# Performance work log

Measured on AMD Instinct MI355X. Metric: run time of the kernel, lower is better.

The kernel has to match this reference:

```python
import jax, jax.numpy as jnp
import numpy as np

B, S, D, N_OPS = 16, 8192, 128, 4


def setup_inputs() -> dict:
    key = jax.random.key(0)
    k1, k2, k3 = jax.random.split(key, 3)
    x = jax.random.normal(k1, (B, S, D), dtype=jnp.float32)
    # candidate op parameters: 4 Linear(D, D) layers, stacked
    W = jax.random.normal(k2, (N_OPS, D, D), dtype=jnp.float32) * (1.0 / np.sqrt(D))
    b = jax.random.normal(k3, (N_OPS, D), dtype=jnp.float32) * 0.01
    # one-hot path selector buffer: weights[0] = 1.0 (as in MixModule.__init__)
    weights = jnp.zeros((N_OPS,), dtype=jnp.float32).at[0].set(1.0)
    return {"x": x, "W": W, "b": b, "weights": weights}


def reference(x, W, b, weights):
    # Faithful to the torch loop: compute EVERY candidate op(x), then the
    # weighted (one-hot) sum. outs: [B, S, n_ops, D]
    outs = jnp.einsum("bsd,ofd->bsof", x, W) + b[None, None, :, :]
    y = jnp.einsum("bsof,o->bsf", outs, weights)
    return y
```

## Files before the change

### kernel.cpp

```cpp
#include <hip/hip_runtime.h>
#include <hip/hip_bf16.h>

#define D 128
#define NOPS 4
#define BS_STRIDE 136
#define ROWS_PER_BLOCK 128

typedef __attribute__((ext_vector_type(8))) short short8;
typedef __attribute__((ext_vector_type(4))) float float4_t;

__global__ void combine_kernel(const float* __restrict__ W,
                               const float* __restrict__ b,
                               const float* __restrict__ wts,
                               __hip_bfloat16* __restrict__ Wc,
                               float* __restrict__ bc) {
    int idx = blockIdx.x * blockDim.x + threadIdx.x;
    float w0 = wts[0], w1 = wts[1], w2 = wts[2], w3 = wts[3];
    if (idx < D * D) {
        float v = w0 * W[idx] + w1 * W[D * D + idx]
                + w2 * W[2 * D * D + idx] + w3 * W[3 * D * D + idx];
        Wc[idx] = __float2bfloat16(v);
    }
    if (idx < D) {
        bc[idx] = w0 * b[idx] + w1 * b[D + idx] + w2 * b[2 * D + idx] + w3 * b[3 * D + idx];
    }
}

__device__ inline short8 cvt8_bf16(float4_t a, float4_t b) {
    union { short8 s; __hip_bfloat16 h[8]; } u;
    u.h[0] = __float2bfloat16(a[0]);
    u.h[1] = __float2bfloat16(a[1]);
    u.h[2] = __float2bfloat16(a[2]);
    u.h[3] = __float2bfloat16(a[3]);
    u.h[4] = __float2bfloat16(b[0]);
    u.h[5] = __float2bfloat16(b[1]);
    u.h[6] = __float2bfloat16(b[2]);
    u.h[7] = __float2bfloat16(b[3]);
    return u.s;
}

__global__ __launch_bounds__(512, 8) void gemm_kernel(const float* __restrict__ x,
                                                      const __hip_bfloat16* __restrict__ Wc,
                                                      const float* __restrict__ bc,
                                                      float* __restrict__ y,
                                                      int M) {
    __shared__ __align__(16) __hip_bfloat16 Bs[D * BS_STRIDE];

    const int tid   = threadIdx.x;
    const int lane  = tid & 63;
    const int wave  = tid >> 6;
    const int wslab = wave >> 1;
    const int whalf = wave & 1;

    #pragma unroll
    for (int i = 0; i < 4; i++) {
        int c  = i * 512 + tid;
        int n  = c >> 4;
        int ko = (c & 15) << 3;
        short8 v = *(const short8*)((const short*)Wc + n * D + ko);
        *(short8*)((short*)Bs + n * BS_STRIDE + ko) = v;
    }
    __syncthreads();

    const int row  = lane & 15;
    const int quad = lane >> 4;

    const int mbase = blockIdx.x * ROWS_PER_BLOCK + wslab * 16 + row;
    if (mbase >= M) return;

    const short* bp0 = (const short*)Bs + (whalf * 64 + row) * BS_STRIDE + quad * 8;

    #pragma unroll
    for (int s = 0; s < 2; s++) {
        const int m = mbase + s * 64;

        const float* xp = x + (size_t)m * D + quad * 8;
        short8 xf[4];
        #pragma unroll
        for (int ks = 0; ks < 4; ks++) {
            float4_t a0 = *(const float4_t*)(xp + ks * 32);
            float4_t a1 = *(const float4_t*)(xp + ks * 32 + 4);
            xf[ks] = cvt8_bf16(a0, a1);
        }

        float4_t acc[4];
        #pragma unroll
        for (int i = 0; i < 4; i++) acc[i] = (float4_t)(0.f);

        #pragma unroll
        for (int ks = 0; ks < 4; ks++) {
            #pragma unroll
            for (int f = 0; f < 4; f++) {
                short8 wfrag = *(const short8*)(bp0 + f * 16 * BS_STRIDE + ks * 32);
                acc[f] = __builtin_amdgcn_mfma_f32_16x16x32_bf16(wfrag, xf[ks], acc[f], 0, 0, 0);
            }
        }

        float* yp = y + (size_t)m * D + whalf * 64 + quad * 4;
        #pragma unroll
        for (int f = 0; f < 4; f++) {
            float4_t bias = *(const float4_t*)(bc + whalf * 64 + f * 16 + quad * 4);
            float4_t out;
            out[0] = acc[f][0] + bias[0];
            out[1] = acc[f][1] + bias[1];
            out[2] = acc[f][2] + bias[2];
            out[3] = acc[f][3] + bias[3];
            __builtin_nontemporal_store(out, (float4_t*)(yp + f * 16));
        }
    }
}

extern "C" void kernel_launch(void* const* d_in, const int* in_sizes, int n_in,
                              void* d_out, int out_size, void* d_ws, size_t ws_size,
                              hipStream_t stream) {
    const float* x   = (const float*)d_in[0];
    const float* W   = (const float*)d_in[1];
    const float* b   = (const float*)d_in[2];
    const float* wts = (const float*)d_in[3];
    float* y = (float*)d_out;

    __hip_bfloat16* Wc = (__hip_bfloat16*)d_ws;
    float* bc = (float*)((char*)d_ws + D * D * sizeof(__hip_bfloat16));

    combine_kernel<<<(D * D + 255) / 256, 256, 0, stream>>>(W, b, wts, Wc, bc);

    const int M = in_sizes[0] / D;
    gemm_kernel<<<M / ROWS_PER_BLOCK, 512, 0, stream>>>(x, Wc, bc, y, M);
}
```

Before: 128.0 us.

## Double-buffer x loads across four row slabs with XOR-swizzled weight LDS

Each block now covers 256 rows in four 64-row slabs per wave pair, prefetching the next slab's fp32 x into registers while the current slab runs its MFMAs. Padded LDS rows are replaced by an XOR swizzle to avoid bank conflicts without extra LDS. Output stores become ordinary stores instead of nontemporal, and launch bounds drop to 4 blocks per CU. The extra register buffers lower occupancy and halve the number of blocks, trading latency hiding by parallelism for explicit prefetch.

```diff
diff --git a/kernel.cpp b/kernel.cpp
--- a/kernel.cpp
+++ b/kernel.cpp
@@ -2,9 +2,8 @@
 #include <hip/hip_bf16.h>
 
 #define D 128
-#define NOPS 4
-#define BS_STRIDE 136
-#define ROWS_PER_BLOCK 128
+#define NSLAB 4
+#define ROWS_PER_BLOCK 256
 
 typedef __attribute__((ext_vector_type(8))) short short8;
 typedef __attribute__((ext_vector_type(4))) float float4_t;
@@ -39,48 +38,68 @@
     return u.s;
 }
 
-__global__ __launch_bounds__(512, 8) void gemm_kernel(const float* __restrict__ x,
+__global__ __launch_bounds__(512, 4) void gemm_kernel(const float* __restrict__ x,
                                                       const __hip_bfloat16* __restrict__ Wc,
                                                       const float* __restrict__ bc,
                                                       float* __restrict__ y,
                                                       int M) {
-    __shared__ __align__(16) __hip_bfloat16 Bs[D * BS_STRIDE];
+    __shared__ __align__(16) __hip_bfloat16 Bs[D * D];
 
     const int tid   = threadIdx.x;
     const int lane  = tid & 63;
     const int wave  = tid >> 6;
     const int wslab = wave >> 1;
     const int whalf = wave & 1;
+    const int r     = lane & 15;
+    const int quad  = lane >> 4;
 
     #pragma unroll
     for (int i = 0; i < 4; i++) {
-        int c  = i * 512 + tid;
-        int n  = c >> 4;
-        int ko = (c & 15) << 3;
-        short8 v = *(const short8*)((const short*)Wc + n * D + ko);
-        *(short8*)((short*)Bs + n * BS_STRIDE + ko) = v;
+        int c = i * 512 + tid;
+        int n = c >> 4;
+        int j = c & 15;
+        short8 v = *(const short8*)((const short*)Wc + n * D + j * 8);
+        *(short8*)((char*)Bs + n * 256 + ((j ^ (n & 15)) << 4)) = v;
     }
+
+    const char* bsBase = (const char*)Bs + (whalf * 64 + r) * 256;
+    int o_[4];
+    #pragma unroll
+    for (int ks = 0; ks < 4; ks++) o_[ks] = (((ks * 4 + quad) ^ r) << 4);
+
     __syncthreads();
 
-    const int row  = lane & 15;
-    const int quad = lane >> 4;
+    if (blockIdx.x * ROWS_PER_BLOCK >= M) return;
 
-    const int mbase = blockIdx.x * ROWS_PER_BLOCK + wslab * 16 + row;
-    if (mbase >= M) return;
+    const int    m0  = blockIdx.x * ROWS_PER_BLOCK + wslab * 16 + r;
+    const float* xp0 = x + (size_t)m0 * D + quad * 8;
 
-    const short* bp0 = (const short*)Bs + (whalf * 64 + row) * BS_STRIDE + quad * 8;
+    float4_t abuf0[8], abuf1[8];
 
     #pragma unroll
-    for (int s = 0; s < 2; s++) {
-        const int m = mbase + s * 64;
+    for (int u = 0; u < 4; u++) {
+        abuf0[2 * u]     = *(const float4_t*)(xp0 + u * 32);
+        abuf0[2 * u + 1] = *(const float4_t*)(xp0 + u * 32 + 4);
+    }
+    #pragma unroll
+    for (int u = 0; u < 4; u++) {
+        abuf1[2 * u]     = *(const float4_t*)(xp0 + 64 * D + u * 32);
+        abuf1[2 * u + 1] = *(const float4_t*)(xp0 + 64 * D + u * 32 + 4);
+    }
 
-        const float* xp = x + (size_t)m * D + quad * 8;
+    auto slab = [&](int s, float4_t (&buf)[8], bool refill) {
         short8 xf[4];
         #pragma unroll
-        for (int ks = 0; ks < 4; ks++) {
-            float4_t a0 = *(const float4_t*)(xp + ks * 32);
-            float4_t a1 = *(const float4_t*)(xp + ks * 32 + 4);
-            xf[ks] = cvt8_bf16(a0, a1);
+        for (int ks = 0; ks < 4; ks++)
+            xf[ks] = cvt8_bf16(buf[2 * ks], buf[2 * ks + 1]);
+
+        if (refill) {
+            const float* xn = xp0 + (size_t)(s + 2) * 64 * D;
+            #pragma unroll
+            for (int u = 0; u < 4; u++) {
+                buf[2 * u]     = *(const float4_t*)(xn + u * 32);
+                buf[2 * u + 1] = *(const float4_t*)(xn + u * 32 + 4);
+            }
         }
 
         float4_t acc[4];
@@ -91,12 +110,12 @@
         for (int ks = 0; ks < 4; ks++) {
             #pragma unroll
             for (int f = 0; f < 4; f++) {
-                short8 wfrag = *(const short8*)(bp0 + f * 16 * BS_STRIDE + ks * 32);
+                short8 wfrag = *(const short8*)(bsBase + f * 4096 + o_[ks]);
                 acc[f] = __builtin_amdgcn_mfma_f32_16x16x32_bf16(wfrag, xf[ks], acc[f], 0, 0, 0);
             }
         }
 
-        float* yp = y + (size_t)m * D + whalf * 64 + quad * 4;
+        float* yp = y + (size_t)(m0 + s * 64) * D + whalf * 64 + quad * 4;
         #pragma unroll
         for (int f = 0; f < 4; f++) {
             float4_t bias = *(const float4_t*)(bc + whalf * 64 + f * 16 + quad * 4);
@@ -105,9 +124,14 @@
             out[1] = acc[f][1] + bias[1];
             out[2] = acc[f][2] + bias[2];
             out[3] = acc[f][3] + bias[3];
-            __builtin_nontemporal_store(out, (float4_t*)(yp + f * 16));
+            *(float4_t*)(yp + f * 16) = out;
         }
-    }
+    };
+
+    slab(0, abuf0, true);
+    slab(1, abuf1, true);
+    slab(2, abuf0, false);
+    slab(3, abuf1, false);
 }
 
 extern "C" void kernel_launch(void* const* d_in, const int* in_sizes, int n_in,
```

New measurement: 132.1 us. +3.2%, slower.
